# Performance work log

Measured on AMD Instinct MI355X. Metric: run time of the kernel, lower is better.

The kernel has to match this reference:

```python
import jax, jax.numpy as jnp
import numpy as np

N, D, W, S = 16384, 256, 64, 8  # utterances, embed dim, attention half-window, speakers


def setup_inputs() -> dict:
    key = jax.random.key(0)
    ks = jax.random.split(key, 8)
    scale = 1.0 / np.sqrt(D)
    return {
        "x": jax.random.normal(ks[0], (N, D), jnp.float32),
        "speaker_ids": jax.random.randint(ks[1], (N,), 0, S, jnp.int32),
        "W_att": jax.random.normal(ks[2], (D, D), jnp.float32) * scale,
        "W_pred": jax.random.normal(ks[3], (D, D), jnp.float32) * scale,
        "W_suc": jax.random.normal(ks[4], (D, D), jnp.float32) * scale,
        "W_same": jax.random.normal(ks[5], (D, D), jnp.float32) * scale,
        "W_diff": jax.random.normal(ks[6], (D, D), jnp.float32) * scale,
    }


def reference(x, speaker_ids, W_att, W_pred, W_suc, W_same, W_diff):
    n = x.shape[0]
    pad = jnp.zeros((W, D), x.dtype)
    # windowed gather: for utterance i, neighbors at offsets [-W, W-1] (2W slots)
    win_idx = jnp.arange(n)[:, None] + jnp.arange(2 * W)[None, :]  # index into padded [N+2W]
    xp = jnp.concatenate([pad, x, pad], axis=0)                    # [N+2W, D]
    windows = xp[win_idx]                                          # [N, 2W, D]
    # raw_attn[i,w] = (edge_att_weights(windows[i,w])) . x[i]
    raw_attn = jnp.einsum("nwd,ed,ne->nw", windows, W_att, x)      # [N, 2W]
    attn = jax.nn.softmax(raw_attn, axis=1)
    # relation masks over the band: j = i + offset
    offs = jnp.arange(2 * W) - W                                   # [-W, W-1]
    j = jnp.arange(n)[:, None] + offs[None, :]                     # [N, 2W]
    valid = (j >= 0) & (j < n)
    jc = jnp.clip(j, 0, n - 1)
    same_spk = speaker_ids[jc] == speaker_ids[:, None]
    masks = [
        valid & (offs >= 0)[None, :],   # pred: edges to current/future within window
        valid & (offs < 0)[None, :],    # suc: edges to past within window
        valid & same_spk,               # same speaker within window
        valid & ~same_spk,              # different speaker within window
    ]
    # relation-specific GCN aggregation: h = sum_r A_r @ (x @ W_r), A_r banded
    h = jnp.zeros_like(x)
    for Wr, m in zip([W_pred, W_suc, W_same, W_diff], masks):
        support = x @ Wr                                           # [N, D]
        sp = jnp.concatenate([pad, support, pad], axis=0)[win_idx]  # [N, 2W, D]
        h = h + jnp.einsum("nw,nwd->nd", attn * m, sp)
    return jax.nn.log_softmax(h, axis=1)
```

## Files before the change

### kernel.cpp

```cpp
#include <hip/hip_runtime.h>
#include <hip/hip_bf16.h>

typedef unsigned short u16;
typedef unsigned int u32;
typedef __attribute__((ext_vector_type(8))) short short8;
typedef __attribute__((ext_vector_type(4))) float floatx4;

#define NU 16384
#define DIM 256
#define AMS 200
#define AC1o 12800u
#define YLO 16896u

#define XHo 0u
#define XLo 4194304u
#define XRo 8388608u
#define ST0 20971520u
#define STROW 16512u
#define STMAT 4227072u
#define WH0o 33652736u
#define WL0o 33718272u
#define WRo  33783808u

__device__ __forceinline__ u16 bfh(float v) {
  return (u16)(__float_as_uint(v) >> 16);
}
__device__ __forceinline__ float bup(u16 u) {
  return __uint_as_float(((u32)u) << 16);
}
__device__ __forceinline__ u16 bfrn(float v) {
  u32 u = __float_as_uint(v);
  return (u16)((u + 0x7fffu + ((u >> 16) & 1u)) >> 16);
}

__global__ __launch_bounds__(256) void prep(
    const float* __restrict__ x,
    const float* __restrict__ wat, const float* __restrict__ wpr,
    const float* __restrict__ wsu, const float* __restrict__ wsm,
    const float* __restrict__ wdf, u16* __restrict__ ws) {
  const int b = blockIdx.x, t = threadIdx.x;
  if (b < 2048) {
    int idx = (b * 256 + t) * 8;
    float4 v0 = *(const float4*)(x + idx);
    float4 v1 = *(const float4*)(x + idx + 4);
    float a[8] = {v0.x, v0.y, v0.z, v0.w, v1.x, v1.y, v1.z, v1.w};
    u16 h[8], l[8], r[8];
#pragma unroll
    for (int q = 0; q < 8; ++q) {
      h[q] = bfh(a[q]);
      l[q] = bfh(a[q] - bup(h[q]));
      r[q] = bfrn(a[q]);
    }
    *(uint4*)(ws + XHo + idx) = *(const uint4*)h;
    *(uint4*)(ws + XLo + idx) = *(const uint4*)l;
    *(uint4*)(ws + XRo + idx) = *(const uint4*)r;
    return;
  }
  const int b2 = b - 2048;
  if (b2 < 32) {
    const int s = b2 & 7, mat = b2 >> 3, n = t;
    const float* Wa = (mat == 0) ? wat : (mat == 1) ? wpr : (mat == 2) ? wsm : wsu;
    const float* Wb = (mat == 0) ? wat : (mat == 1) ? wsu : (mat == 2) ? wdf : wdf;
    const float c1  = (mat == 0) ? 0.f : (mat == 3) ? 1.f : -1.f;
    u16 hbuf[32], lbuf[32];
#pragma unroll 8
    for (int k = 0; k < 32; ++k) {
      float v = Wa[(s * 32 + k) * 256 + n] + c1 * Wb[(s * 32 + k) * 256 + n];
      if (mat == 0) { hbuf[k] = bfh(v); lbuf[k] = bfh(v - bup(hbuf[k])); }
      else          { hbuf[k] = bfrn(v); }
    }
    u16* dh = ws + ((mat == 0) ? WH0o : (WRo + (size_t)(mat - 1) * 65536))
               + (size_t)s * 8192 + n * 32;
#pragma unroll
    for (int p = 0; p < 4; ++p) *(uint4*)(dh + p * 8) = ((const uint4*)hbuf)[p];
    if (mat == 0) {
      u16* dl = ws + WL0o + (size_t)s * 8192 + n * 32;
#pragma unroll
      for (int p = 0; p < 4; ++p) *(uint4*)(dl + p * 8) = ((const uint4*)lbuf)[p];
    }
  } else {
    int g = (b2 - 32) * 256 + t;
    int r = g >> 13, rem = g & 8191;
    int d = rem >> 5, p = rem & 31;
    size_t base = ST0 + (size_t)r * STMAT + (size_t)d * STROW;
    size_t off = (p < 16) ? (base + p * 4) : (base + 16448 + (p - 16) * 4);
    *(ushort4*)(ws + off) = make_ushort4(0, 0, 0, 0);
  }
}

__global__ __launch_bounds__(512, 4) void gemmS1(u16* __restrict__ ws) {
  __shared__ __align__(16) u16 U[39168];

  const int t = threadIdx.x, row0 = blockIdx.x * 32;
  const int w = t >> 6, ln = t & 15, quad = (t & 63) >> 4, q8 = quad * 8;
  const int n0 = w * 32;

#pragma unroll
  for (int cc = 0; cc < 2; ++cc) {
    int idx = t + 512 * cc;
    int row = idx >> 5, c8 = (idx & 31) * 8;
    *(uint4*)(U + row * 264 + c8) =
        *(const uint4*)(ws + XRo + (size_t)(row0 + row) * 256 + c8);
  }
  __syncthreads();

  floatx4 acc[3][2][2];
#pragma unroll
  for (int mat = 0; mat < 3; ++mat)
#pragma unroll
    for (int m = 0; m < 2; ++m)
#pragma unroll
      for (int nt = 0; nt < 2; ++nt) acc[mat][m][nt] = (floatx4){0.f, 0.f, 0.f, 0.f};

  for (int s = 0; s < 8; ++s) {
    short8 ah[2];
#pragma unroll
    for (int m = 0; m < 2; ++m)
      ah[m] = *(const short8*)(U + (m * 16 + ln) * 264 + s * 32 + q8);
#pragma unroll
    for (int mat = 0; mat < 3; ++mat) {
      short8 bh[2];
#pragma unroll
      for (int nt = 0; nt < 2; ++nt)
        bh[nt] = *(const short8*)(ws + WRo + (size_t)mat * 65536
                                  + (size_t)s * 8192 + (n0 + nt * 16 + ln) * 32 + q8);
#pragma unroll
      for (int m = 0; m < 2; ++m)
#pragma unroll
        for (int nt = 0; nt < 2; ++nt)
          acc[mat][m][nt] = __builtin_amdgcn_mfma_f32_16x16x32_bf16(ah[m], bh[nt], acc[mat][m][nt], 0, 0, 0);
    }
  }

#pragma unroll
  for (int mat = 0; mat < 3; ++mat)
#pragma unroll
    for (int m = 0; m < 2; ++m)
#pragma unroll
      for (int nt = 0; nt < 2; ++nt) {
        int col = n0 + nt * 16 + ln;
        ushort4 pk = make_ushort4(bfrn(acc[mat][m][nt][0]), bfrn(acc[mat][m][nt][1]),
                                  bfrn(acc[mat][m][nt][2]), bfrn(acc[mat][m][nt][3]));
        *(ushort4*)(U + 8448 + mat * 10240 + col * 40 + m * 16 + quad * 4) = pk;
      }
  __syncthreads();

#pragma unroll
  for (int mat = 0; mat < 3; ++mat)
#pragma unroll
    for (int cc = 0; cc < 2; ++cc) {
      int c = t + 512 * cc;
      int d = c >> 2, part = c & 3;
      *(uint4*)(ws + ST0 + (size_t)mat * STMAT + (size_t)d * STROW + 64 + row0 + part * 8) =
          *(const uint4*)(U + 8448 + mat * 10240 + d * 40 + part * 8);
    }
}

__global__ __launch_bounds__(512, 2) void fused_attn(
    const u16* __restrict__ ws, const int* __restrict__ spk,
    float* __restrict__ out)
{
  __shared__ __align__(16) u16 U[33792];
  __shared__ int spkw[192];
  __shared__ float prt[64][2], prs[64][2];
  __shared__ float red[64][8];

  const int t    = threadIdx.x;
  const int w    = t >> 6;
  const int ln   = t & 15;
  const int quad = (t & 63) >> 4;
  const int q8   = quad * 8;
  const int bswz = (blockIdx.x & 7) * 32 + (blockIdx.x >> 3);
  const int i0   = bswz * 64;
  const int mw   = w & 3;
  const int half = w >> 2;
  const int n0   = w * 32;

  if (t < 192) spkw[t] = spk[min(max(i0 - 64 + t, 0), NU - 1)];

  {
#pragma unroll
    for (int cc = 0; cc < 8; ++cc) {
      int idx = t + 512 * cc;
      int buf = idx >> 11, e = idx & 2047;
      int row = e >> 5, c8 = (e & 31) * 8;
      *(uint4*)(U + buf * YLO + row * 264 + c8) =
          *(const uint4*)(ws + (buf ? XLo : XHo) + (size_t)(i0 + row) * 256 + c8);
    }
    __syncthreads();

    floatx4 acc[4][2];
#pragma unroll
    for (int m = 0; m < 4; ++m)
#pragma unroll
      for (int nt = 0; nt < 2; ++nt) acc[m][nt] = (floatx4){0.f, 0.f, 0.f, 0.f};

    for (int s = 0; s < 8; ++s) {
      short8 ah[4], al[4];
#pragma unroll
      for (int m = 0; m < 4; ++m) {
        ah[m] = *(const short8*)(U + (m * 16 + ln) * 264 + s * 32 + q8);
        al[m] = *(const short8*)(U + YLO + (m * 16 + ln) * 264 + s * 32 + q8);
      }
      short8 bh[2], bl[2];
#pragma unroll
      for (int nt = 0; nt < 2; ++nt) {
        size_t off = (size_t)s * 8192 + (n0 + nt * 16 + ln) * 32 + q8;
        bh[nt] = *(const short8*)(ws + WH0o + off);
        bl[nt] = *(const short8*)(ws + WL0o + off);
      }
#pragma unroll
      for (int m = 0; m < 4; ++m)
#pragma unroll
        for (int nt = 0; nt < 2; ++nt) {
          acc[m][nt] = __builtin_amdgcn_mfma_f32_16x16x32_bf16(ah[m], bh[nt], acc[m][nt], 0, 0, 0);
          acc[m][nt] = __builtin_amdgcn_mfma_f32_16x16x32_bf16(ah[m], bl[nt], acc[m][nt], 0, 0, 0);
          acc[m][nt] = __builtin_amdgcn_mfma_f32_16x16x32_bf16(al[m], bh[nt], acc[m][nt], 0, 0, 0);
        }
    }
    __syncthreads();

#pragma unroll
    for (int m = 0; m < 4; ++m)
#pragma unroll
      for (int nt = 0; nt < 2; ++nt) {
        int col = n0 + nt * 16 + ln;
#pragma unroll
        for (int r = 0; r < 4; ++r) {
          int row = m * 16 + quad * 4 + r;
          float y = acc[m][nt][r];
          u16 hh = bfh(y);
          U[row * 264 + col] = hh;
          U[YLO + row * 264 + col] = bfh(y - bup(hh));
        }
      }
  }
  __syncthreads();

  floatx4 accP[6];
#pragma unroll
  for (int cc = 0; cc < 6; ++cc) accP[cc] = (floatx4){0.f, 0.f, 0.f, 0.f};

  u32 jro[6];
#pragma unroll
  for (int cc = 0; cc < 6; ++cc) {
    int xrow = half * 96 + cc * 16 + ln;
    int jc = min(max(i0 + xrow - 64, 0), NU - 1);
    jro[cc] = (u32)jc * 256u + (u32)q8;
  }

#pragma unroll 2
  for (int ks = 0; ks < 8; ++ks) {
    const u16* yb = U + (mw * 16 + ln) * 264 + ks * 32 + q8;
    short8 yh8 = *(const short8*)yb;
    short8 yl8 = *(const short8*)(yb + YLO);
#pragma unroll
    for (int cc = 0; cc < 6; ++cc) {
      short8 xbh = *(const short8*)(ws + XHo + jro[cc] + ks * 32);
      short8 xbl = *(const short8*)(ws + XLo + jro[cc] + ks * 32);
      accP[cc] = __builtin_amdgcn_mfma_f32_16x16x32_bf16(yh8, xbh, accP[cc], 0, 0, 0);
      accP[cc] = __builtin_amdgcn_mfma_f32_16x16x32_bf16(yh8, xbl, accP[cc], 0, 0, 0);
      accP[cc] = __builtin_amdgcn_mfma_f32_16x16x32_bf16(yl8, xbh, accP[cc], 0, 0, 0);
    }
  }

  int  c_of[6];
  bool vj[6];
#pragma unroll
  for (int cc = 0; cc < 6; ++cc) {
    c_of[cc] = half * 96 + cc * 16 + ln;
    int j = i0 + c_of[cc] - 64;
    vj[cc] = (j >= 0) && (j < NU);
  }
#pragma unroll
  for (int r = 0; r < 4; ++r) {
    int row = mw * 16 + quad * 4 + r;
    float mx = -3.4e38f;
#pragma unroll
    for (int cc = 0; cc < 6; ++cc) {
      int rel = c_of[cc] - row;
      bool inb = (rel >= 0) && (rel < 128);
      if (inb) mx = fmaxf(mx, vj[cc] ? accP[cc][r] : 0.f);
    }
#pragma unroll
    for (int o = 1; o < 16; o <<= 1) mx = fmaxf(mx, __shfl_xor(mx, o));
    if (ln == 0) prt[row][half] = mx;
  }
  __syncthreads();
#pragma unroll
  for (int r = 0; r < 4; ++r) {
    int row = mw * 16 + quad * 4 + r;
    float gm = fmaxf(prt[row][0], prt[row][1]);
    float s = 0.f;
#pragma unroll
    for (int cc = 0; cc < 6; ++cc) {
      int rel = c_of[cc] - row;
      bool inb = (rel >= 0) && (rel < 128);
      float vv = vj[cc] ? accP[cc][r] : 0.f;
      float e  = inb ? __expf(vv - gm) : 0.f;
      s += e;
      accP[cc][r] = (inb && vj[cc]) ? e : 0.f;
    }
#pragma unroll
    for (int o = 1; o < 16; o <<= 1) s += __shfl_xor(s, o);
    if (ln == 0) prs[row][half] = s;
  }
  __syncthreads();
#pragma unroll
  for (int r = 0; r < 4; ++r) {
    int row = mw * 16 + quad * 4 + r;
    float inv = 1.f / (prs[row][0] + prs[row][1]);
#pragma unroll
    for (int cc = 0; cc < 6; ++cc)
      U[row * AMS + c_of[cc]] = bfrn(accP[cc][r] * inv);
  }
  __syncthreads();

  {
    const int arow = t >> 3, aseg = t & 7;
    const int sr = spkw[arow + 64];
    const int cb = aseg * 24;
#pragma unroll
    for (int p = 0; p < 6; ++p) {
      ushort4 av = *(const ushort4*)(U + arow * AMS + cb + p * 4);
      u16 aq[4] = {av.x, av.y, av.z, av.w};
      u16 b1v[4];
#pragma unroll
      for (int q = 0; q < 4; ++q) {
        int c = cb + p * 4 + q;
        b1v[q] = (spkw[c] == sr) ? aq[q] : (u16)0;
      }
      *(ushort4*)(U + AC1o + arow * AMS + cb + p * 4) = *(const ushort4*)b1v;
    }
  }
  __syncthreads();

  floatx4 acc2[4][2];
#pragma unroll
  for (int m = 0; m < 4; ++m)
#pragma unroll
    for (int nt = 0; nt < 2; ++nt) acc2[m][nt] = (floatx4){0.f, 0.f, 0.f, 0.f};

#pragma unroll
  for (int kj = 0; kj < 6; ++kj) {
    short8 af[4], af1[4];
#pragma unroll
    for (int m = 0; m < 4; ++m) {
      af[m]  = *(const short8*)(U + (m * 16 + ln) * AMS + kj * 32 + q8);
      af1[m] = *(const short8*)(U + AC1o + (m * 16 + ln) * AMS + kj * 32 + q8);
    }
    size_t sb[2];
#pragma unroll
    for (int nt = 0; nt < 2; ++nt)
      sb[nt] = (size_t)ST0 + (size_t)(n0 + nt * 16 + ln) * STROW
             + (size_t)(i0 + kj * 32) + q8;
#pragma unroll
    for (int nt = 0; nt < 2; ++nt) {
      short8 b2 = *(const short8*)(ws + sb[nt] + 2 * (size_t)STMAT);
      short8 b1 = *(const short8*)(ws + sb[nt] + 1 * (size_t)STMAT);
#pragma unroll
      for (int m = 0; m < 4; ++m) {
        acc2[m][nt] = __builtin_amdgcn_mfma_f32_16x16x32_bf16(af[m],  b2, acc2[m][nt], 0, 0, 0);
        acc2[m][nt] = __builtin_amdgcn_mfma_f32_16x16x32_bf16(af1[m], b1, acc2[m][nt], 0, 0, 0);
      }
    }
    if (kj >= 2) {
      short8 a0m[4];
#pragma unroll
      for (int m = 0; m < 4; ++m) {
        a0m[m] = af[m];
        if (!(32 * kj >= 16 * m + 79)) {
          int tthr = m * 16 + ln + 64 - kj * 32 - q8;
#pragma unroll
          for (int e = 0; e < 8; ++e)
            if (e < tthr) a0m[m][e] = 0;
        }
      }
#pragma unroll
      for (int nt = 0; nt < 2; ++nt) {
        short8 b0 = *(const short8*)(ws + sb[nt]);
#pragma unroll
        for (int m = 0; m < 4; ++m) {
          if (32 * kj < 16 * m + 33) continue;
          acc2[m][nt] = __builtin_amdgcn_mfma_f32_16x16x32_bf16(a0m[m], b0, acc2[m][nt], 0, 0, 0);
        }
      }
    }
  }

#pragma unroll
  for (int m = 0; m < 4; ++m)
#pragma unroll
    for (int r = 0; r < 4; ++r) {
      float v = fmaxf(acc2[m][0][r], acc2[m][1][r]);
#pragma unroll
      for (int o = 1; o < 16; o <<= 1) v = fmaxf(v, __shfl_xor(v, o));
      if (ln == 0) red[m * 16 + quad * 4 + r][w] = v;
    }
  __syncthreads();
  float gmx[4][4];
#pragma unroll
  for (int m = 0; m < 4; ++m)
#pragma unroll
    for (int r = 0; r < 4; ++r) {
      int row = m * 16 + quad * 4 + r;
      float g = red[row][0];
#pragma unroll
      for (int ww = 1; ww < 8; ++ww) g = fmaxf(g, red[row][ww]);
      gmx[m][r] = g;
    }
  __syncthreads();
#pragma unroll
  for (int m = 0; m < 4; ++m)
#pragma unroll
    for (int r = 0; r < 4; ++r) {
      float e = __expf(acc2[m][0][r] - gmx[m][r]) + __expf(acc2[m][1][r] - gmx[m][r]);
#pragma unroll
      for (int o = 1; o < 16; o <<= 1) e += __shfl_xor(e, o);
      if (ln == 0) red[m * 16 + quad * 4 + r][w] = e;
    }
  __syncthreads();
#pragma unroll
  for (int m = 0; m < 4; ++m)
#pragma unroll
    for (int r = 0; r < 4; ++r) {
      int row = m * 16 + quad * 4 + r;
      float s = red[row][0];
#pragma unroll
      for (int ww = 1; ww < 8; ++ww) s += red[row][ww];
      float lse = gmx[m][r] + logf(s);
      size_t rowg = (size_t)(i0 + row) * DIM;
      out[rowg + n0 + ln]      = acc2[m][0][r] - lse;
      out[rowg + n0 + 16 + ln] = acc2[m][1][r] - lse;
    }
}

extern "C" void kernel_launch(void* const* d_in, const int* in_sizes, int n_in,
                              void* d_out, int out_size, void* d_ws, size_t ws_size,
                              hipStream_t stream) {
  const float* x   = (const float*)d_in[0];
  const int*   spk = (const int*)d_in[1];
  const float* wat = (const float*)d_in[2];
  const float* wpr = (const float*)d_in[3];
  const float* wsu = (const float*)d_in[4];
  const float* wsm = (const float*)d_in[5];
  const float* wdf = (const float*)d_in[6];
  float* out = (float*)d_out;
  u16* ws = (u16*)d_ws;

  hipLaunchKernelGGL(prep, dim3(2176), dim3(256), 0, stream,
                     x, wat, wpr, wsu, wsm, wdf, ws);
  hipLaunchKernelGGL(gemmS1, dim3(512), dim3(512), 0, stream, ws);
  hipLaunchKernelGGL(fused_attn, dim3(256), dim3(512), 0, stream, ws, spk, out);
}
```

Baseline: 160.7 us.

## Stage X hi/lo tiles into swizzled LDS double buffer via global_load_lds

The neighbour-row X hi/lo bf16 tiles are now copied into a double-buffered LDS staging area with direct global-to-LDS loads, one k-slice ahead of the MFMA loop. Before, every wave read those tiles from global memory itself, even though the four waves sharing a row block read the same rows. The staging uses an XOR swizzle on 16-byte slots to avoid LDS bank conflicts, and adds a barrier per k-step. LDS use grows and the launch-bound hint of two blocks per CU is dropped, which may lower occupancy.

```diff
diff --git a/kernel.cpp b/kernel.cpp
--- a/kernel.cpp
+++ b/kernel.cpp
@@ -11,6 +11,7 @@
 #define AMS 200
 #define AC1o 12800u
 #define YLO 16896u
+#define STGo 33792u
 
 #define XHo 0u
 #define XLo 4194304u
@@ -31,6 +32,12 @@
 __device__ __forceinline__ u16 bfrn(float v) {
   u32 u = __float_as_uint(v);
   return (u16)((u + 0x7fffu + ((u >> 16) & 1u)) >> 16);
+}
+
+__device__ __forceinline__ void gload16(const u16* g, u16* l) {
+  __builtin_amdgcn_global_load_lds(
+      (__attribute__((address_space(1))) void*)(uintptr_t)g,
+      (__attribute__((address_space(3))) void*)(uintptr_t)l, 16, 0, 0);
 }
 
 __global__ __launch_bounds__(256) void prep(
@@ -156,11 +163,11 @@
     }
 }
 
-__global__ __launch_bounds__(512, 2) void fused_attn(
+__global__ __launch_bounds__(512) void fused_attn(
     const u16* __restrict__ ws, const int* __restrict__ spk,
     float* __restrict__ out)
 {
-  __shared__ __align__(16) u16 U[33792];
+  __shared__ __align__(16) u16 U[58368];
   __shared__ int spkw[192];
   __shared__ float prt[64][2], prs[64][2];
   __shared__ float red[64][8];
@@ -235,33 +242,49 @@
         }
       }
   }
-  __syncthreads();
+
+  auto STAGE = [&](int ks, int par) {
+    const int kd = ks * 32;
+    u16* db = U + STGo + par * 12288;
+#pragma unroll
+    for (int cc = 0; cc < 3; ++cc) {
+      int idx  = t + 512 * cc;
+      int bsel = (idx >= 768) ? 1 : 0;
+      int e    = idx - bsel * 768;
+      int row  = e >> 2, s = e & 3;
+      int sw   = s ^ ((row >> 1) & 3);
+      int jc   = min(max(i0 + row - 64, 0), NU - 1);
+      const u16* src = ws + (bsel ? XLo : XHo) + (size_t)jc * 256 + kd + sw * 8;
+      u16* dst = db + bsel * 6144 + e * 8;
+      gload16(src, dst);
+    }
+  };
 
   floatx4 accP[6];
 #pragma unroll
   for (int cc = 0; cc < 6; ++cc) accP[cc] = (floatx4){0.f, 0.f, 0.f, 0.f};
 
-  u32 jro[6];
-#pragma unroll
-  for (int cc = 0; cc < 6; ++cc) {
-    int xrow = half * 96 + cc * 16 + ln;
-    int jc = min(max(i0 + xrow - 64, 0), NU - 1);
-    jro[cc] = (u32)jc * 256u + (u32)q8;
-  }
-
-#pragma unroll 2
+  STAGE(0, 0);
+  __syncthreads();
+#pragma unroll
   for (int ks = 0; ks < 8; ++ks) {
+    if (ks < 7) STAGE(ks + 1, (ks + 1) & 1);
+    const u16* sp = U + STGo + (ks & 1) * 12288;
     const u16* yb = U + (mw * 16 + ln) * 264 + ks * 32 + q8;
     short8 yh8 = *(const short8*)yb;
     short8 yl8 = *(const short8*)(yb + YLO);
 #pragma unroll
     for (int cc = 0; cc < 6; ++cc) {
-      short8 xbh = *(const short8*)(ws + XHo + jro[cc] + ks * 32);
-      short8 xbl = *(const short8*)(ws + XLo + jro[cc] + ks * 32);
+      int xrow = half * 96 + cc * 16 + ln;
+      int slot = quad ^ ((xrow >> 1) & 3);
+      const u16* xb = sp + xrow * 32 + slot * 8;
+      short8 xbh = *(const short8*)xb;
+      short8 xbl = *(const short8*)(xb + 6144);
       accP[cc] = __builtin_amdgcn_mfma_f32_16x16x32_bf16(yh8, xbh, accP[cc], 0, 0, 0);
       accP[cc] = __builtin_amdgcn_mfma_f32_16x16x32_bf16(yh8, xbl, accP[cc], 0, 0, 0);
       accP[cc] = __builtin_amdgcn_mfma_f32_16x16x32_bf16(yl8, xbh, accP[cc], 0, 0, 0);
     }
+    __syncthreads();
   }
 
   int  c_of[6];
```

New measurement: 144.1 us, median of 3. 10.4% less time.
